# Optimization experiments

Measured on AMD Instinct MI355X. Metric: run time of the kernel, lower is better.

## Reference

```python
import jax, jax.numpy as jnp
import numpy as np

N = 50000          # nodes
E = 800000         # edges (avg degree 16)
DIN = 128          # d_input
H = 8              # heads per layer
D = 16             # per-head hidden dim
HID = H * D        # 128
ALPHA = 0.2        # LeakyReLU negative slope in GAT attention
BN_EPS = 1e-5


def _xavier(key, shape):
    fan_in, fan_out = shape[0], shape[-1]
    lim = np.sqrt(6.0 / (fan_in + fan_out)).astype(np.float32)
    return jax.random.uniform(key, shape, jnp.float32, -lim, lim)


def setup_inputs() -> dict:
    key = jax.random.key(0)
    ks = jax.random.split(key, 8)
    x = jax.random.normal(ks[0], (N, DIN), jnp.float32)
    edge_idx = jax.random.randint(ks[1], (2, E), 0, N)
    W1 = _xavier(ks[2], (DIN, HID))
    a1 = _xavier(ks[3], (H, 2 * D))
    W2 = _xavier(ks[4], (HID, HID))
    a2 = _xavier(ks[5], (H, 2 * D))
    W3 = _xavier(ks[6], (HID, HID))
    a3 = _xavier(ks[7], (H, 2 * D))
    ones = jnp.ones((HID,), jnp.float32)
    zeros = jnp.zeros((HID,), jnp.float32)
    return {"x": x, "edge_idx": edge_idx,
            "W1": W1, "a1": a1, "W2": W2, "a2": a2, "W3": W3, "a3": a3,
            "g1": ones, "b1": zeros, "g2": ones, "b2": zeros, "g3": ones, "b3": zeros}


def _leaky(x):
    return jnp.where(x >= 0, x, ALPHA * x)


def _gat_layer(x, src, dst, W, a):
    # x: [N, Fin]; W: [Fin, H*D]; a: [H, 2D]
    h = (x @ W).reshape(-1, H, D)                       # [N, H, D]
    e_src = jnp.einsum('nhd,hd->nh', h, a[:, :D])       # a^T part for source node
    e_dst = jnp.einsum('nhd,hd->nh', h, a[:, D:])       # a^T part for destination node
    e = _leaky(e_src[src] + e_dst[dst])                 # [E, H]
    m = jax.ops.segment_max(e, dst, num_segments=N)     # per-dst stable softmax max
    m = jnp.where(jnp.isfinite(m), m, 0.0)              # empty segments -> 0
    w = jnp.exp(e - m[dst])                             # [E, H]
    den = jax.ops.segment_sum(w, dst, num_segments=N)   # [N, H]
    agg = jax.ops.segment_sum(h[src] * w[:, :, None], dst, num_segments=N)  # [N, H, D]
    out = agg / (den[:, :, None] + 1e-16)
    return out.reshape(-1, HID)                         # concat heads


def _bn(x, g, b):
    # BatchNorm1d training-mode math over the node axis
    mu = x.mean(axis=0)
    var = x.var(axis=0)
    return g * (x - mu) * jax.lax.rsqrt(var + BN_EPS) + b


def reference(x, edge_idx, W1, a1, W2, a2, W3, a3, g1, b1, g2, b2, g3, b3):
    src, dst = edge_idx[0], edge_idx[1]
    h1 = jax.nn.elu(_bn(_gat_layer(x, src, dst, W1, a1), g1, b1))
    h2 = jax.nn.elu(_bn(_gat_layer(h1, src, dst, W2, a2), g2, b2))
    h3_in = h1 + h2  # skip connection
    return _bn(_gat_layer(h3_in, src, dst, W3, a3), g3, b3)
```

## Files before the change

kernel.cpp:

```cpp
#include <hip/hip_runtime.h>
#include <hip/hip_bf16.h>
#include <hip/hip_fp16.h>
#include <cstddef>

#define NNODES 50000
#define NEDGES 800000
#define HID 128
#define NHEAD 8
#define AGG_NB (NNODES / 16)
#define NSLICE 64
#define SLAYER (NSLICE * 512)

#define NBUCK 196
#define BCH 2048
#define BIN_NB ((NEDGES + BCH - 1) / BCH)

typedef __attribute__((ext_vector_type(4))) float floatx4;
typedef _Float16 __attribute__((ext_vector_type(8))) half8;
typedef _Float16 __attribute__((ext_vector_type(2))) half2v;

static inline size_t align_up(size_t x, size_t a) { return (x + a - 1) & ~(a - 1); }

__device__ inline float fexp2(float x) {
#if __has_builtin(__builtin_amdgcn_exp2f)
    return __builtin_amdgcn_exp2f(x);
#else
    return __expf(x * 0.69314718055994531f);
#endif
}

__device__ inline unsigned short f2h(float f) {
    return __builtin_bit_cast(unsigned short, (_Float16)f);
}

__global__ __launch_bounds__(256) void init_kernel(const float* __restrict__ W1,
                                                   const float* __restrict__ W2,
                                                   const float* __restrict__ W3,
                                                   unsigned short* __restrict__ Wt,
                                                   int* __restrict__ zeroA, int nA,
                                                   float* __restrict__ zeroB, int nB) {
    int b = blockIdx.x;
    int t = threadIdx.x;
    if (b < 192) {
        int layer = b >> 6;
        const float* W = (layer == 0) ? W1 : ((layer == 1) ? W2 : W3);
        int idx = (b & 63) * 256 + t;
        int n = idx & 127;
        int k = idx >> 7;
        Wt[layer * 16384 + n * 128 + k] = f2h(W[idx]);
    } else {
        int nb = gridDim.x - 192;
        int bb = b - 192;
        for (int i = bb * 256 + t; i < nA; i += nb * 256) zeroA[i] = 0;
        for (int i = bb * 256 + t; i < nB; i += nb * 256) zeroB[i] = 0.f;
    }
}

__global__ __launch_bounds__(256) void bin_count_kernel(const int* __restrict__ edge,
                                                        int* __restrict__ bucketCnt) {
    __shared__ int h[NBUCK];
    int t = threadIdx.x;
    if (t < NBUCK) h[t] = 0;
    __syncthreads();
    for (int i = blockIdx.x * 256 + t; i < NEDGES; i += gridDim.x * 256)
        atomicAdd(&h[edge[NEDGES + i] >> 8], 1);
    __syncthreads();
    if (t < NBUCK && h[t]) atomicAdd(&bucketCnt[t], h[t]);
}

__global__ __launch_bounds__(256) void bin_scatter_kernel(const int* __restrict__ edge,
                                                          const int* __restrict__ bucketCnt,
                                                          int* __restrict__ bucketCursor,
                                                          unsigned int* __restrict__ binned) {
    __shared__ int sA[256];
    __shared__ int hcnt[NBUCK];
    __shared__ int hbase[NBUCK];
    __shared__ int gbase[NBUCK];
    __shared__ unsigned int sEnt[BCH];
    __shared__ unsigned char sBk[BCH];
    int t = threadIdx.x;
    int e0 = blockIdx.x * BCH;
    int nv = NEDGES - e0;
    if (nv > BCH) nv = BCH;

    int gcnt = (t < NBUCK) ? bucketCnt[t] : 0;
    sA[t] = gcnt;
    __syncthreads();
    for (int off = 1; off < 256; off <<= 1) {
        int x = (t >= off) ? sA[t - off] : 0;
        __syncthreads();
        sA[t] += x;
        __syncthreads();
    }
    int gExBase = sA[t] - gcnt;
    if (t < NBUCK) hcnt[t] = 0;
    __syncthreads();

    int myB[8];
    int myR[8];
    unsigned int myP[8];
    #pragma unroll
    for (int j = 0; j < 8; ++j) {
        int idx = j * 256 + t;
        myB[j] = -1;
        if (idx < nv) {
            int s = edge[e0 + idx];
            int d = edge[NEDGES + e0 + idx];
            int bk = d >> 8;
            myB[j] = bk;
            myP[j] = (unsigned)s | ((unsigned)(d & 255) << 16);
            myR[j] = atomicAdd(&hcnt[bk], 1);
        }
    }
    __syncthreads();
    int hc = (t < NBUCK) ? hcnt[t] : 0;
    sA[t] = hc;
    __syncthreads();
    for (int off = 1; off < 256; off <<= 1) {
        int x = (t >= off) ? sA[t - off] : 0;
        __syncthreads();
        sA[t] += x;
        __syncthreads();
    }
    if (t < NBUCK) {
        hbase[t] = sA[t] - hc;
        gbase[t] = gExBase + atomicAdd(&bucketCursor[t], hc);
    }
    __syncthreads();
    #pragma unroll
    for (int j = 0; j < 8; ++j) {
        if (myB[j] >= 0) {
            int p = hbase[myB[j]] + myR[j];
            sEnt[p] = myP[j];
            sBk[p] = (unsigned char)myB[j];
        }
    }
    __syncthreads();
    #pragma unroll
    for (int j = 0; j < 8; ++j) {
        int i = j * 256 + t;
        if (i < nv) {
            int bk = sBk[i];
            binned[gbase[bk] + (i - hbase[bk])] = sEnt[i];
        }
    }
}

__global__ __launch_bounds__(256) void fine_csr_kernel(const int* __restrict__ bucketCnt,
                                                       const unsigned int* __restrict__ binned,
                                                       int* __restrict__ offs,
                                                       int* __restrict__ csr) {
    __shared__ int sA[256];
    __shared__ int sB[256];
    int t = threadIdx.x;
    int b = blockIdx.x;
    int v = (t < NBUCK) ? bucketCnt[t] : 0;
    sA[t] = v;
    __syncthreads();
    for (int off = 1; off < 256; off <<= 1) {
        int x = (t >= off) ? sA[t - off] : 0;
        __syncthreads();
        sA[t] += x;
        __syncthreads();
    }
    int cntb = bucketCnt[b];
    int base = sA[b] - cntb;
    sB[t] = 0;
    __syncthreads();
    for (int i = t; i < cntb; i += 256)
        atomicAdd(&sB[(binned[base + i] >> 16) & 255], 1);
    __syncthreads();
    int nc = sB[t];
    sA[t] = nc;
    __syncthreads();
    for (int off = 1; off < 256; off <<= 1) {
        int x = (t >= off) ? sA[t - off] : 0;
        __syncthreads();
        sA[t] += x;
        __syncthreads();
    }
    int nodeBase = base + sA[t] - nc;
    int gid = b * 256 + t;
    if (gid < NNODES) offs[gid] = nodeBase;
    if (b == NBUCK - 1 && t == 0) offs[NNODES] = NEDGES;
    sB[t] = nodeBase;
    __syncthreads();
    for (int i = t; i < cntb; i += 256) {
        unsigned e = binned[base + i];
        int pos = atomicAdd(&sB[(e >> 16) & 255], 1);
        csr[pos] = (int)(e & 0xFFFFu);
    }
}

__global__ __launch_bounds__(256) void bn_finalize_kernel(const float* __restrict__ statsPart,
                                                          const float* __restrict__ g,
                                                          const float* __restrict__ b,
                                                          float* __restrict__ ssv) {
    __shared__ float sm[256];
    int t = threadIdx.x;
    const float* base = statsPart + (t & 127) + ((t >> 7) << 7);
    float s = 0.f;
    #pragma unroll 8
    for (int k = 0; k < NSLICE; ++k) s += base[k * 512];
    sm[t] = s;
    __syncthreads();
    if (t < 128) {
        float mu = sm[t] / (float)NNODES;
        float var = sm[128 + t] / (float)NNODES - mu * mu;
        float rstd = rsqrtf(var + 1e-5f);
        float scale = g[t] * rstd;
        ssv[t] = scale;
        ssv[128 + t] = b[t] - mu * scale;
    }
}

#define GROWS 64
#define ASTRIDE 136
#define LOG2E 1.4426950408889634f
__global__ __launch_bounds__(256) void gemm_kernel(const float* __restrict__ Xin,
                                                   const float* __restrict__ skip,
                                                   const float* __restrict__ ssv,
                                                   const unsigned short* __restrict__ Wt,
                                                   const float* __restrict__ a,
                                                   float* __restrict__ Hw,
                                                   unsigned short* __restrict__ Hb,
                                                   float* __restrict__ esrc,
                                                   float* __restrict__ edst,
                                                   int mode) {
    __shared__ unsigned short As[GROWS * ASTRIDE];
    __shared__ unsigned short Bs[128 * ASTRIDE];
    int tid = threadIdx.x;
    int rowBase = blockIdx.x * GROWS;

    uint4 breg[8];
    #pragma unroll
    for (int q = 0; q < 8; ++q) {
        int i = q * 256 + tid;
        breg[q] = *(const uint4*)(Wt + (i >> 4) * 128 + (i & 15) * 8);
    }

    int r = tid >> 2;
    int cs = (tid & 3) * 32;
    int gr = rowBase + r;
    bool valid = gr < NNODES;
    float4 vv[8];
    if (valid) {
        #pragma unroll
        for (int j = 0; j < 8; ++j)
            vv[j] = *(const float4*)(Xin + (size_t)gr * HID + cs + j * 4);
    } else {
        #pragma unroll
        for (int j = 0; j < 8; ++j) vv[j] = make_float4(0.f, 0.f, 0.f, 0.f);
    }

    #pragma unroll
    for (int q = 0; q < 8; ++q) {
        int i = q * 256 + tid;
        *(uint4*)(&Bs[(i >> 4) * ASTRIDE + (i & 15) * 8]) = breg[q];
    }

    if (mode >= 1 && valid) {
        #pragma unroll
        for (int j = 0; j < 8; ++j) {
            int ch = cs + j * 4;
            float4 sc = *(const float4*)(ssv + ch);
            float4 sh = *(const float4*)(ssv + 128 + ch);
            float4 v = vv[j];
            v.x = sc.x * v.x + sh.x;
            v.y = sc.y * v.y + sh.y;
            v.z = sc.z * v.z + sh.z;
            v.w = sc.w * v.w + sh.w;
            v.x = (v.x > 0.f) ? v.x : expm1f(v.x);
            v.y = (v.y > 0.f) ? v.y : expm1f(v.y);
            v.z = (v.z > 0.f) ? v.z : expm1f(v.z);
            v.w = (v.w > 0.f) ? v.w : expm1f(v.w);
            if (mode == 2) {
                float4 s = *(const float4*)(skip + (size_t)gr * HID + ch);
                v.x += s.x; v.y += s.y; v.z += s.z; v.w += s.w;
            }
            vv[j] = v;
        }
        if (mode == 1) {
            #pragma unroll
            for (int j = 0; j < 8; ++j)
                *(float4*)(Hw + (size_t)gr * HID + cs + j * 4) = vv[j];
        }
    }
    {
        unsigned int pk[16];
        #pragma unroll
        for (int j = 0; j < 8; ++j) {
            pk[2 * j]     = __builtin_bit_cast(unsigned int,
                                __builtin_amdgcn_cvt_pkrtz(vv[j].x, vv[j].y));
            pk[2 * j + 1] = __builtin_bit_cast(unsigned int,
                                __builtin_amdgcn_cvt_pkrtz(vv[j].z, vv[j].w));
        }
        #pragma unroll
        for (int q = 0; q < 4; ++q)
            *(uint4*)(&As[r * ASTRIDE + cs + q * 8]) =
                make_uint4(pk[4 * q], pk[4 * q + 1], pk[4 * q + 2], pk[4 * q + 3]);
    }

    __syncthreads();

    int wv = tid >> 6;
    int lane = tid & 63;
    int l15 = lane & 15;
    int quad = lane >> 4;
    const unsigned short* Arow = &As[(wv * 16 + l15) * ASTRIDE + quad * 8];
    half8 af[4];
    #pragma unroll
    for (int c = 0; c < 4; ++c) af[c] = *(const half8*)(Arow + c * 32);

    floatx4 acc[8];
    #pragma unroll
    for (int h = 0; h < 8; ++h) {
        acc[h] = (floatx4){0.f, 0.f, 0.f, 0.f};
        const unsigned short* Brow = &Bs[(h * 16 + l15) * ASTRIDE + quad * 8];
        #pragma unroll
        for (int c = 0; c < 4; ++c) {
            half8 bfr = *(const half8*)(Brow + c * 32);
            acc[h] = __builtin_amdgcn_mfma_f32_16x16x32_f16(af[c], bfr, acc[h], 0, 0, 0);
        }
    }

    #pragma unroll
    for (int h = 0; h < 8; ++h) {
        #pragma unroll
        for (int reg = 0; reg < 4; ++reg)
            As[(wv * 16 + quad * 4 + reg) * ASTRIDE + h * 16 + l15] = f2h(acc[h][reg]);
    }

    {
        int rr = tid >> 2;
        int hp = tid & 3;
        int grr = rowBase + rr;
        const unsigned short* row = &As[rr * ASTRIDE + hp * 32];
        uint4 u[4];
        #pragma unroll
        for (int q = 0; q < 4; ++q) u[q] = *(const uint4*)(row + q * 8);
        if (grr < NNODES) {
            uint4* dst = (uint4*)(Hb + (size_t)grr * HID + hp * 32);
            #pragma unroll
            for (int q = 0; q < 4; ++q) dst[q] = u[q];
            float f[32];
            #pragma unroll
            for (int q = 0; q < 4; ++q) {
                unsigned int* pu = (unsigned int*)&u[q];
                #pragma unroll
                for (int j = 0; j < 4; ++j) {
                    half2v hv = __builtin_bit_cast(half2v, pu[j]);
                    f[q * 8 + 2 * j]     = (float)hv[0];
                    f[q * 8 + 2 * j + 1] = (float)hv[1];
                }
            }
            int h0 = hp * 2, h1 = hp * 2 + 1;
            float es0 = 0.f, ev0 = 0.f, es1 = 0.f, ev1 = 0.f;
            #pragma unroll
            for (int j = 0; j < 16; ++j) {
                es0 += f[j] * a[h0 * 32 + j];
                ev0 += f[j] * a[h0 * 32 + 16 + j];
                es1 += f[16 + j] * a[h1 * 32 + j];
                ev1 += f[16 + j] * a[h1 * 32 + 16 + j];
            }
            esrc[grr * NHEAD + h0] = es0 * LOG2E;
            esrc[grr * NHEAD + h1] = es1 * LOG2E;
            edst[grr * NHEAD + h0] = ev0 * LOG2E;
            edst[grr * NHEAD + h1] = ev1 * LOG2E;
        }
    }
}

__global__ __launch_bounds__(256) void aggregate_kernel(const int* __restrict__ offs,
                                                        const int* __restrict__ csr,
                                                        const float* __restrict__ esrc,
                                                        const float* __restrict__ edst,
                                                        const unsigned int* __restrict__ Hb,
                                                        float* __restrict__ out,
                                                        float* __restrict__ statsPart) {
    int tid = threadIdx.x;
    int wv = tid >> 6;
    int lane = tid & 63;
    int grp = lane >> 4;
    int sub = lane & 15;
    int head = sub >> 1;
    int n = blockIdx.x * 16 + wv * 4 + grp;
    int beg = offs[n], end = offs[n + 1];
    float ed = edst[n * NHEAD + head];
    float acc[8];
    #pragma unroll
    for (int q = 0; q < 8; ++q) acc[q] = 0.f;
    float den = 0.f;
    for (int i = beg; i < end; i += 4) {
        int ss[4];
        #pragma unroll
        for (int j = 0; j < 4; ++j)
            ss[j] = csr[min(i + j, end - 1)];
        float ee[4];
        uint4 hh[4];
        #pragma unroll
        for (int j = 0; j < 4; ++j)
            ee[j] = esrc[(unsigned)ss[j] * 8u + (unsigned)head];
        #pragma unroll
        for (int j = 0; j < 4; ++j)
            hh[j] = *(const uint4*)(Hb + (unsigned)ss[j] * 64u + (unsigned)sub * 4u);
        #pragma unroll
        for (int j = 0; j < 4; ++j) {
            float e = ee[j] + ed;
            e = fmaxf(e, 0.2f * e);
            float w = fexp2(e);
            w = (i + j < end) ? w : 0.f;
            den += w;
            half2v h0 = __builtin_bit_cast(half2v, hh[j].x);
            half2v h1 = __builtin_bit_cast(half2v, hh[j].y);
            half2v h2 = __builtin_bit_cast(half2v, hh[j].z);
            half2v h3 = __builtin_bit_cast(half2v, hh[j].w);
            acc[0] += w * (float)h0[0];
            acc[1] += w * (float)h0[1];
            acc[2] += w * (float)h1[0];
            acc[3] += w * (float)h1[1];
            acc[4] += w * (float)h2[0];
            acc[5] += w * (float)h2[1];
            acc[6] += w * (float)h3[0];
            acc[7] += w * (float)h3[1];
        }
    }
    float inv = 1.f / (den + 1e-16f);
    float4 o0 = make_float4(acc[0] * inv, acc[1] * inv, acc[2] * inv, acc[3] * inv);
    float4 o1 = make_float4(acc[4] * inv, acc[5] * inv, acc[6] * inv, acc[7] * inv);
    float* orow = out + (size_t)n * HID + sub * 8;
    *(float4*)orow = o0;
    *(float4*)(orow + 4) = o1;

    __shared__ float sm[16 * 136];
    float* srow = &sm[(wv * 4 + grp) * 136 + sub * 8];
    *(float4*)srow = o0;
    *(float4*)(srow + 4) = o1;
    __syncthreads();
    if (tid < 128) {
        float s = 0.f, s2 = 0.f;
        #pragma unroll
        for (int rr = 0; rr < 16; ++rr) {
            float v = sm[rr * 136 + tid];
            s += v;
            s2 += v * v;
        }
        float* slice = statsPart + (blockIdx.x & (NSLICE - 1)) * 512;
        atomicAdd(&slice[tid], s);
        atomicAdd(&slice[128 + tid], s2);
    }
}

__global__ __launch_bounds__(256) void final_apply_kernel(const float* __restrict__ X,
                                                          const float* __restrict__ ssv,
                                                          float* __restrict__ out) {
    __shared__ float ssm[256];
    int tid = threadIdx.x;
    ssm[tid] = ssv[tid];
    __syncthreads();
    int total4 = NNODES * HID / 4;
    for (int i = blockIdx.x * 256 + tid; i < total4; i += gridDim.x * 256) {
        float4 v = ((const float4*)X)[i];
        int c4 = (i & 31) * 4;
        float4 sc = *(const float4*)(ssm + c4);
        float4 sh = *(const float4*)(ssm + 128 + c4);
        v.x = sc.x * v.x + sh.x;
        v.y = sc.y * v.y + sh.y;
        v.z = sc.z * v.z + sh.z;
        v.w = sc.w * v.w + sh.w;
        ((float4*)out)[i] = v;
    }
}

extern "C" void kernel_launch(void* const* d_in, const int* in_sizes, int n_in,
                              void* d_out, int out_size, void* d_ws, size_t ws_size,
                              hipStream_t stream) {
    const float* x   = (const float*)d_in[0];
    const int* edge  = (const int*)d_in[1];
    const float* W1  = (const float*)d_in[2];
    const float* a1  = (const float*)d_in[3];
    const float* W2  = (const float*)d_in[4];
    const float* a2  = (const float*)d_in[5];
    const float* W3  = (const float*)d_in[6];
    const float* a3  = (const float*)d_in[7];
    const float* g1  = (const float*)d_in[8];
    const float* b1  = (const float*)d_in[9];
    const float* g2  = (const float*)d_in[10];
    const float* b2  = (const float*)d_in[11];
    const float* g3  = (const float*)d_in[12];
    const float* b3  = (const float*)d_in[13];
    float* outp      = (float*)d_out;

    char* p = (char*)d_ws;
    size_t cur = 0;
    auto carve = [&](size_t bytes) {
        void* r = p + cur;
        cur = align_up(cur + bytes, 256);
        return r;
    };
    int*   offs   = (int*)carve((NNODES + 1) * sizeof(int));
    int*   csr    = (int*)carve(NEDGES * sizeof(int));
    unsigned short* wt = (unsigned short*)carve(3 * 16384 * sizeof(unsigned short));
    unsigned short* hb = (unsigned short*)carve((size_t)NNODES * HID * sizeof(unsigned short));
    float* agg    = (float*)carve((size_t)NNODES * HID * sizeof(float));
    float* h1     = (float*)carve((size_t)NNODES * HID * sizeof(float));
    float* esrc   = (float*)carve((size_t)NNODES * NHEAD * sizeof(float));
    float* edst   = (float*)carve((size_t)NNODES * NHEAD * sizeof(float));
    float* stats  = (float*)carve(3 * SLAYER * sizeof(float));
    int*   bcnt   = (int*)carve(2 * NBUCK * sizeof(int));
    int*   bcur   = bcnt + NBUCK;
    float* ssv    = (float*)carve(3 * 256 * sizeof(float));
    float* stats1 = stats;
    float* stats2 = stats + SLAYER;
    float* stats3 = stats + 2 * SLAYER;
    float* ssv1 = ssv;
    float* ssv2 = ssv + 256;
    float* ssv3 = ssv + 512;
    unsigned int* binned = (unsigned int*)h1;

    const int GB = (NNODES + GROWS - 1) / GROWS;

    init_kernel<<<256, 256, 0, stream>>>(W1, W2, W3, wt,
                                         bcnt, 2 * NBUCK,
                                         stats, 3 * SLAYER);
    bin_count_kernel<<<256, 256, 0, stream>>>(edge, bcnt);
    bin_scatter_kernel<<<BIN_NB, 256, 0, stream>>>(edge, bcnt, bcur, binned);
    fine_csr_kernel<<<NBUCK, 256, 0, stream>>>(bcnt, binned, offs, csr);

    gemm_kernel<<<GB, 256, 0, stream>>>(x, nullptr, nullptr,
                                        wt, a1, nullptr, hb, esrc, edst, 0);
    aggregate_kernel<<<AGG_NB, 256, 0, stream>>>(offs, csr, esrc, edst,
                                                 (const unsigned int*)hb, agg, stats1);
    bn_finalize_kernel<<<1, 256, 0, stream>>>(stats1, g1, b1, ssv1);

    gemm_kernel<<<GB, 256, 0, stream>>>(agg, nullptr, ssv1,
                                        wt + 16384, a2, h1, hb, esrc, edst, 1);
    aggregate_kernel<<<AGG_NB, 256, 0, stream>>>(offs, csr, esrc, edst,
                                                 (const unsigned int*)hb, agg, stats2);
    bn_finalize_kernel<<<1, 256, 0, stream>>>(stats2, g2, b2, ssv2);

    gemm_kernel<<<GB, 256, 0, stream>>>(agg, h1, ssv2,
                                        wt + 32768, a3, nullptr, hb, esrc, edst, 2);
    aggregate_kernel<<<AGG_NB, 256, 0, stream>>>(offs, csr, esrc, edst,
                                                 (const unsigned int*)hb, agg, stats3);
    bn_finalize_kernel<<<1, 256, 0, stream>>>(stats3, g3, b3, ssv3);

    final_apply_kernel<<<768, 256, 0, stream>>>(agg, ssv3, outp);
}
```

Before: 360.4 us.

## Hoist bucket prefix scan into one kernel; read GEMM weights from global

Adds a single-block bucket_scan_kernel that computes bucket base offsets once, so the 391 bin_scatter blocks and 196 fine_csr blocks no longer each redo a 256-wide shared-memory scan. In the GEMM, the weight tile is no longer staged in shared memory: MFMA B fragments are loaded directly from global (L2/L1-cached) weights. This drops the 34 KB Bs buffer and one barrier, and a launch-bounds hint of 4 blocks per SIMD is added to raise occupancy. The cost is one extra tiny kernel launch and repeated uncoalesced-ish global loads of weights per wave instead of shared reuse.

```diff
diff --git a/kernel.cpp b/kernel.cpp
--- a/kernel.cpp
+++ b/kernel.cpp
@@ -68,8 +68,25 @@
     if (t < NBUCK && h[t]) atomicAdd(&bucketCnt[t], h[t]);
 }
 
+__global__ __launch_bounds__(256) void bucket_scan_kernel(const int* __restrict__ bucketCnt,
+                                                          int* __restrict__ bucketBase) {
+    __shared__ int sA[256];
+    int t = threadIdx.x;
+    int v = (t < NBUCK) ? bucketCnt[t] : 0;
+    sA[t] = v;
+    __syncthreads();
+    for (int off = 1; off < 256; off <<= 1) {
+        int x = (t >= off) ? sA[t - off] : 0;
+        __syncthreads();
+        sA[t] += x;
+        __syncthreads();
+    }
+    if (t < NBUCK) bucketBase[t] = sA[t] - v;
+    if (t == 0) bucketBase[NBUCK] = NEDGES;
+}
+
 __global__ __launch_bounds__(256) void bin_scatter_kernel(const int* __restrict__ edge,
-                                                          const int* __restrict__ bucketCnt,
+                                                          const int* __restrict__ bucketBase,
                                                           int* __restrict__ bucketCursor,
                                                           unsigned int* __restrict__ binned) {
     __shared__ int sA[256];
@@ -83,16 +100,6 @@
     int nv = NEDGES - e0;
     if (nv > BCH) nv = BCH;
 
-    int gcnt = (t < NBUCK) ? bucketCnt[t] : 0;
-    sA[t] = gcnt;
-    __syncthreads();
-    for (int off = 1; off < 256; off <<= 1) {
-        int x = (t >= off) ? sA[t - off] : 0;
-        __syncthreads();
-        sA[t] += x;
-        __syncthreads();
-    }
-    int gExBase = sA[t] - gcnt;
     if (t < NBUCK) hcnt[t] = 0;
     __syncthreads();
 
@@ -124,7 +131,7 @@
     }
     if (t < NBUCK) {
         hbase[t] = sA[t] - hc;
-        gbase[t] = gExBase + atomicAdd(&bucketCursor[t], hc);
+        gbase[t] = bucketBase[t] + atomicAdd(&bucketCursor[t], hc);
     }
     __syncthreads();
     #pragma unroll
@@ -147,6 +154,7 @@
 }
 
 __global__ __launch_bounds__(256) void fine_csr_kernel(const int* __restrict__ bucketCnt,
+                                                       const int* __restrict__ bucketBase,
                                                        const unsigned int* __restrict__ binned,
                                                        int* __restrict__ offs,
                                                        int* __restrict__ csr) {
@@ -154,17 +162,8 @@
     __shared__ int sB[256];
     int t = threadIdx.x;
     int b = blockIdx.x;
-    int v = (t < NBUCK) ? bucketCnt[t] : 0;
-    sA[t] = v;
-    __syncthreads();
-    for (int off = 1; off < 256; off <<= 1) {
-        int x = (t >= off) ? sA[t - off] : 0;
-        __syncthreads();
-        sA[t] += x;
-        __syncthreads();
-    }
     int cntb = bucketCnt[b];
-    int base = sA[b] - cntb;
+    int base = bucketBase[b];
     sB[t] = 0;
     __syncthreads();
     for (int i = t; i < cntb; i += 256)
@@ -217,27 +216,19 @@
 #define GROWS 64
 #define ASTRIDE 136
 #define LOG2E 1.4426950408889634f
-__global__ __launch_bounds__(256) void gemm_kernel(const float* __restrict__ Xin,
-                                                   const float* __restrict__ skip,
-                                                   const float* __restrict__ ssv,
-                                                   const unsigned short* __restrict__ Wt,
-                                                   const float* __restrict__ a,
-                                                   float* __restrict__ Hw,
-                                                   unsigned short* __restrict__ Hb,
-                                                   float* __restrict__ esrc,
-                                                   float* __restrict__ edst,
-                                                   int mode) {
+__global__ __launch_bounds__(256, 4) void gemm_kernel(const float* __restrict__ Xin,
+                                                      const float* __restrict__ skip,
+                                                      const float* __restrict__ ssv,
+                                                      const unsigned short* __restrict__ Wt,
+                                                      const float* __restrict__ a,
+                                                      float* __restrict__ Hw,
+                                                      unsigned short* __restrict__ Hb,
+                                                      float* __restrict__ esrc,
+                                                      float* __restrict__ edst,
+                                                      int mode) {
     __shared__ unsigned short As[GROWS * ASTRIDE];
-    __shared__ unsigned short Bs[128 * ASTRIDE];
     int tid = threadIdx.x;
     int rowBase = blockIdx.x * GROWS;
-
-    uint4 breg[8];
-    #pragma unroll
-    for (int q = 0; q < 8; ++q) {
-        int i = q * 256 + tid;
-        breg[q] = *(const uint4*)(Wt + (i >> 4) * 128 + (i & 15) * 8);
-    }
 
     int r = tid >> 2;
     int cs = (tid & 3) * 32;
@@ -251,12 +242,6 @@
     } else {
         #pragma unroll
         for (int j = 0; j < 8; ++j) vv[j] = make_float4(0.f, 0.f, 0.f, 0.f);
-    }
-
-    #pragma unroll
-    for (int q = 0; q < 8; ++q) {
-        int i = q * 256 + tid;
-        *(uint4*)(&Bs[(i >> 4) * ASTRIDE + (i & 15) * 8]) = breg[q];
     }
 
     if (mode >= 1 && valid) {
@@ -301,8 +286,6 @@
                 make_uint4(pk[4 * q], pk[4 * q + 1], pk[4 * q + 2], pk[4 * q + 3]);
     }
 
-    __syncthreads();
-
     int wv = tid >> 6;
     int lane = tid & 63;
     int l15 = lane & 15;
@@ -316,7 +299,7 @@
     #pragma unroll
     for (int h = 0; h < 8; ++h) {
         acc[h] = (floatx4){0.f, 0.f, 0.f, 0.f};
-        const unsigned short* Brow = &Bs[(h * 16 + l15) * ASTRIDE + quad * 8];
+        const unsigned short* Brow = Wt + (h * 16 + l15) * 128 + quad * 8;
         #pragma unroll
         for (int c = 0; c < 4; ++c) {
             half8 bfr = *(const half8*)(Brow + c * 32);
@@ -507,8 +490,9 @@
     float* esrc   = (float*)carve((size_t)NNODES * NHEAD * sizeof(float));
     float* edst   = (float*)carve((size_t)NNODES * NHEAD * sizeof(float));
     float* stats  = (float*)carve(3 * SLAYER * sizeof(float));
-    int*   bcnt   = (int*)carve(2 * NBUCK * sizeof(int));
+    int*   bcnt   = (int*)carve((3 * NBUCK + 1) * sizeof(int));
     int*   bcur   = bcnt + NBUCK;
+    int*   bbase  = bcnt + 2 * NBUCK;
     float* ssv    = (float*)carve(3 * 256 * sizeof(float));
     float* stats1 = stats;
     float* stats2 = stats + SLAYER;
@@ -524,8 +508,9 @@
                                          bcnt, 2 * NBUCK,
                                          stats, 3 * SLAYER);
     bin_count_kernel<<<256, 256, 0, stream>>>(edge, bcnt);
-    bin_scatter_kernel<<<BIN_NB, 256, 0, stream>>>(edge, bcnt, bcur, binned);
-    fine_csr_kernel<<<NBUCK, 256, 0, stream>>>(bcnt, binned, offs, csr);
+    bucket_scan_kernel<<<1, 256, 0, stream>>>(bcnt, bbase);
+    bin_scatter_kernel<<<BIN_NB, 256, 0, stream>>>(edge, bbase, bcur, binned);
+    fine_csr_kernel<<<NBUCK, 256, 0, stream>>>(bcnt, bbase, binned, offs, csr);
 
     gemm_kernel<<<GB, 256, 0, stream>>>(x, nullptr, nullptr,
                                         wt, a1, nullptr, hb, esrc, edst, 0);
```

Result: slower. 407.1 us (+13.0%).
